# Kernel optimization log

Measured on AMD Instinct MI355X. Metric: run time of the kernel, lower is better.

Reference implementation:

```python
import jax, jax.numpy as jnp
import numpy as np
from jax import lax

# ---- config (matches init_kwargs / detectron2-style inference defaults) ----
B, R, K = 8, 2000, 80          # images, proposals per image, foreground classes
H, W = 800.0, 1333.0           # image (height, width) used for box clipping
SCORE_THRESH = 0.05
NMS_THRESH = 0.5
M = 2048                        # fixed NMS candidate budget (pre-NMS top_k)
T = 100                         # topk_per_image


def setup_inputs() -> dict:
    key = jax.random.key(0)
    k1, k2, k3, k4, k5 = jax.random.split(key, 5)
    # well-formed proposal boxes (x1, y1, x2, y2)
    cx = jax.random.uniform(k1, (B, R)) * W
    cy = jax.random.uniform(k2, (B, R)) * H
    bw = jax.random.uniform(k3, (B, R)) * 300.0 + 2.0
    bh = jax.random.uniform(k4, (B, R)) * 300.0 + 2.0
    boxes = jnp.stack([cx - bw / 2, cy - bh / 2, cx + bw / 2, cy + bh / 2], axis=-1)
    k5a, k5b = jax.random.split(k5)
    scores = jax.random.uniform(k5a, (B, R, K + 1))          # (R, K+1), last col = bg
    bases = jax.random.normal(k5b, (B, R, 7)) * 0.1          # 6 base deltas + 1 h delta
    return {"boxes": boxes.astype(jnp.float32),
            "scores": scores.astype(jnp.float32),
            "bases": bases.astype(jnp.float32)}


def _delta_to_bases(bs, bx):
    # bs: (T, 6) deltas, bx: (T, 4) boxes -> (T, 10) polygon + midpoint
    firstx, firsty = bs[:, 2], bs[:, 3]
    secondx, secondy = bs[:, 4], bs[:, 5]
    x1, y1, x2, y2 = bx[:, 0], bx[:, 1], bx[:, 2], bx[:, 3]
    dx = x2 - x1
    dy = y2 - y1
    midx = (x1 + x2) / 2 + bs[:, 0] * dx
    midy = (y1 + y2) / 2 + bs[:, 1] * dy
    px1 = midx + firstx * dx
    py1 = midy + firsty * dy
    px2 = midx + secondx * dx
    py2 = midy + secondy * dy
    px3 = midx - secondx * dx
    py3 = midy - secondy * dy
    px4 = midx - firstx * dx
    py4 = midy - firsty * dy
    return jnp.stack((px1, py1, px2, py2, px3, py3, px4, py4, midx, midy), axis=-1)


def _delta_to_h(dh, bx):
    dy = bx[:, 3] - bx[:, 1]
    return dy + dh * dy


def _pairwise_iou(b):
    # b: (M, 4). Only used inside a boolean comparison -> no grad path, as in torch NMS.
    x1, y1, x2, y2 = b[:, 0], b[:, 1], b[:, 2], b[:, 3]
    area = jnp.clip(x2 - x1, 0) * jnp.clip(y2 - y1, 0)
    xx1 = jnp.maximum(x1[:, None], x1[None, :])
    yy1 = jnp.maximum(y1[:, None], y1[None, :])
    xx2 = jnp.minimum(x2[:, None], x2[None, :])
    yy2 = jnp.minimum(y2[:, None], y2[None, :])
    inter = jnp.clip(xx2 - xx1, 0) * jnp.clip(yy2 - yy1, 0)
    return inter / (area[:, None] + area[None, :] - inter + 1e-7)


def _single_image(boxes, scores, bases):
    finite = jnp.all(jnp.isfinite(boxes), axis=1) & jnp.all(jnp.isfinite(scores), axis=1)
    scores_k = scores[:, :-1]                                 # drop background (R,K)
    # Boxes.clip(image_shape)
    boxes = jnp.stack([jnp.clip(boxes[:, 0], 0.0, W),
                       jnp.clip(boxes[:, 1], 0.0, H),
                       jnp.clip(boxes[:, 2], 0.0, W),
                       jnp.clip(boxes[:, 3], 0.0, H)], axis=-1)
    # score threshold -> flat (R*K) candidate list, fixed-size top_k selection
    flat = jnp.where(finite[:, None] & (scores_k > SCORE_THRESH), scores_k, -jnp.inf)
    top_scores, top_idx = lax.top_k(flat.reshape(R * K), M)   # (M,)
    box_idx = top_idx // K
    cls = top_idx % K
    cboxes = boxes[box_idx]                                   # (M,4)
    cbases = bases[box_idx]                                   # (M,7)
    valid = jnp.isfinite(top_scores)
    # batched_nms: offset boxes per class so cross-class IoU = 0
    off = (cls.astype(boxes.dtype) * (jnp.maximum(H, W) + 2.0))[:, None]
    iou = _pairwise_iou(cboxes + off)                         # (M,M)

    def body(i, st):
        keep, supp = st
        ki = valid[i] & jnp.logical_not(supp[i])
        keep = keep.at[i].set(ki)
        supp = supp | (ki & (iou[i] > NMS_THRESH))
        return keep, supp

    keep, _ = lax.fori_loop(0, M, body,
                            (jnp.zeros((M,), bool), jnp.zeros((M,), bool)))
    masked = jnp.where(keep, top_scores, -jnp.inf)
    fscores, sel = lax.top_k(masked, T)                       # keep[:topk_per_image]
    fvalid = jnp.isfinite(fscores)
    fscores = jnp.where(fvalid, fscores, 0.0)
    fboxes = cboxes[sel] * fvalid[:, None]
    fbases = cbases[sel]
    fcls = jnp.where(fvalid, cls[sel], -1)
    h = _delta_to_h(fbases[:, 6], fboxes) * fvalid            # (T,)
    dec = _delta_to_bases(fbases[:, 0:6], fboxes) * fvalid[:, None]  # (T,10)
    return dec, h, fboxes, fscores, fcls, fvalid


def reference(boxes, scores, bases):
    # returns per-image padded detections:
    # pred_bases (B,T,10), pred_h (B,T), pred_boxes (B,T,4), scores (B,T),
    # pred_classes (B,T) int, valid mask (B,T)
    return jax.vmap(_single_image)(boxes, scores, bases)
```

## Files before the change

kernel.cpp:

```cpp
#include <hip/hip_runtime.h>
#include <stdint.h>

using u64 = unsigned long long;
using u32 = unsigned;

namespace {
constexpr int RR = 2000;
constexpr int KK = 80;
constexpr int KS = 81;
constexpr int BB = 8;
constexpr int MM = 2048;
constexpr int TT = 100;
constexpr int NB = 2048;
constexpr int CAP = 4096;
constexpr int SPLIT = 50;
constexpr int RPB = RR / SPLIT;
constexpr int FPB = RPB * KS;
constexpr int V4  = FPB / 4;
constexpr int CPB = RPB * KK;
constexpr int SPLIT_H = 10;
constexpr int RPB_H = RR / SPLIT_H;
constexpr int FPB_H = RPB_H * KS;
constexpr int V4_H  = FPB_H / 4;
constexpr float WW  = 1333.0f;
constexpr float HH  = 800.0f;
constexpr float OFF = 1335.0f;
constexpr float STH = 0.05f;
constexpr float NMS = 0.5f;

constexpr size_t HIST_OFF   = 0;
constexpr size_t CNT_OFF    = 65536;
constexpr size_t ZERO_BYTES = 65568;
constexpr size_t CSTAR_OFF  = 65568;
constexpr size_t ROWOK_OFF  = 65664;
constexpr size_t CAND_OFF   = 81920;
}

__global__ __launch_bounds__(1024) void k_hist(const float* __restrict__ boxes,
                                               const float* __restrict__ scores,
                                               u32* __restrict__ hist_g,
                                               unsigned char* __restrict__ rowok_g) {
    const int b = blockIdx.x / SPLIT_H, sb = blockIdx.x % SPLIT_H, tid = threadIdx.x;
    const int r0 = sb * RPB_H;
    const float4* sv = (const float4*)(scores + (size_t)b * RR * KS + (size_t)r0 * KS);
    __shared__ u32 bad[RPB_H];
    __shared__ u32 h[NB];

    const int q0 = tid, q1 = tid + 1024, q2 = tid + 2048, q3 = tid + 3072;
    const float4 v0 = sv[q0];
    const float4 v1 = sv[q1];
    const float4 v2 = sv[q2];
    const float4 v3 = (q3 < V4_H) ? sv[q3] : make_float4(0.f, 0.f, 0.f, 0.f);

    if (tid < RPB_H) bad[tid] = 0;
    for (int i = tid; i < NB; i += 1024) h[i] = 0;
    __syncthreads();

    if (tid < RPB_H) {
        const float4 bx = ((const float4*)(boxes + (size_t)b * RR * 4))[r0 + tid];
        if (!(isfinite(bx.x) && isfinite(bx.y) && isfinite(bx.z) && isfinite(bx.w)))
            atomicOr(&bad[tid], 1u);
    }
    auto chk = [&](int q, const float4& v) {
        if (q < V4_H) {
            const int i0 = 4 * q;
            if (!isfinite(v.x)) atomicOr(&bad[(i0    ) / KS], 1u);
            if (!isfinite(v.y)) atomicOr(&bad[(i0 + 1) / KS], 1u);
            if (!isfinite(v.z)) atomicOr(&bad[(i0 + 2) / KS], 1u);
            if (!isfinite(v.w)) atomicOr(&bad[(i0 + 3) / KS], 1u);
        }
    };
    chk(q0, v0); chk(q1, v1); chk(q2, v2); chk(q3, v3);
    __syncthreads();
    if (tid < RPB_H) rowok_g[b * RR + r0 + tid] = bad[tid] ? 0 : 1;

    auto acc = [&](int idx, float s) {
        const int r_l = idx / KS, k = idx - r_l * KS;
        if (k < KK && bad[r_l] == 0 && s > STH) {
            int bk = (int)(s * (float)NB);
            bk = min(max(bk, 0), NB - 1);
            atomicAdd(&h[bk], 1u);
        }
    };
    auto accv = [&](int q, const float4& v) {
        if (q < V4_H) {
            const int i0 = 4 * q;
            acc(i0, v.x); acc(i0 + 1, v.y); acc(i0 + 2, v.z); acc(i0 + 3, v.w);
        }
    };
    accv(q0, v0); accv(q1, v1); accv(q2, v2); accv(q3, v3);
    __syncthreads();
    for (int i = tid; i < NB; i += 1024)
        if (h[i]) atomicAdd(&hist_g[b * NB + i], h[i]);
}

__global__ __launch_bounds__(256) void k_cut(const u32* __restrict__ hist_g,
                                             u32* __restrict__ cstar_g) {
    const int b = blockIdx.x, tid = threadIdx.x;
    __shared__ u32 h[NB];
    __shared__ u32 cs[256];
    __shared__ u32 cstar_s;
    for (int i = tid; i < NB; i += 256) h[i] = hist_g[b * NB + i];
    if (tid == 0) cstar_s = 0;
    __syncthreads();

    u32 loc[8];
    const int hi = NB - 1 - 8 * tid;
    u32 sum = 0;
#pragma unroll
    for (int j = 0; j < 8; ++j) { loc[j] = h[hi - j]; sum += loc[j]; }
    cs[tid] = sum;
    __syncthreads();
    for (int s = 1; s < 256; s <<= 1) {
        const u32 t = (tid >= s) ? cs[tid - s] : 0u;
        __syncthreads();
        cs[tid] += t;
        __syncthreads();
    }
    const u32 P = cs[tid], Pm1 = (tid > 0) ? cs[tid - 1] : 0u;
    if (P >= (u32)MM && Pm1 < (u32)MM) {
        u32 run = Pm1;
#pragma unroll
        for (int j = 0; j < 8; ++j) {
            run += loc[j];
            if (run >= (u32)MM) { cstar_s = (u32)(hi - j); break; }
        }
    }
    __syncthreads();
    if (tid == 0) cstar_g[b] = cstar_s;
}

__global__ __launch_bounds__(256) void k_compact(const float* __restrict__ scores,
                                                 const u32* __restrict__ cstar_g,
                                                 const unsigned char* __restrict__ rowok_g,
                                                 u64* __restrict__ cand,
                                                 u32* __restrict__ cnt_g) {
    const int b = blockIdx.x / SPLIT, sb = blockIdx.x % SPLIT, tid = threadIdx.x;
    const int r0 = sb * RPB;
    const float4* sv = (const float4*)(scores + (size_t)b * RR * KS + (size_t)r0 * KS);
    __shared__ u64 stage[CPB];
    __shared__ u32 rok[RPB];
    __shared__ u32 scnt, base_s;
    if (tid < RPB) rok[tid] = rowok_g[b * RR + r0 + tid];
    if (tid == 0) scnt = 0;
    __syncthreads();
    const u32 cstar = cstar_g[b];

    auto put = [&](int idx, float s) {
        const int r_l = idx / KS, k = idx - r_l * KS;
        if (k < KK && rok[r_l] && s > STH) {
            int bk = (int)(s * (float)NB);
            bk = min(max(bk, 0), NB - 1);
            if ((u32)bk >= cstar) {
                const u32 p = atomicAdd(&scnt, 1u);
                const u32 eg = (u32)((r0 + r_l) * KK + k);
                stage[p] = ((u64)__float_as_uint(s) << 32) | (u32)(~eg);
            }
        }
    };
#pragma unroll
    for (int it = 0; it < 4; ++it) {
        const int q = tid + it * 256;
        if (q < V4) {
            const float4 v = sv[q];
            const int i0 = 4 * q;
            put(i0, v.x); put(i0 + 1, v.y); put(i0 + 2, v.z); put(i0 + 3, v.w);
        }
    }
    __syncthreads();
    if (tid == 0) base_s = atomicAdd(&cnt_g[b], scnt);
    __syncthreads();
    const u32 base = base_s, nn = scnt;
    u64* cb = cand + (size_t)b * CAP;
    for (u32 i = tid; i < nn; i += 256) {
        const u32 pos = base + i;
        if (pos < (u32)CAP) cb[pos] = stage[i];
    }
}

__device__ __forceinline__ void cmpsw(u64& a, u64& b, bool desc) {
    const u64 mx = a > b ? a : b, mn = a > b ? b : a;
    a = desc ? mx : mn;
    b = desc ? mn : mx;
}
template <unsigned KQ, unsigned JQ>
__device__ __forceinline__ void shfl_stage(u64 (&val)[4], int lane) {
#pragma unroll
    for (int r = 0; r < 4; ++r) {
        const unsigned v = (unsigned)(r * 64 + lane);
        const u64 pv = __shfl_xor(val[r], (int)JQ, 64);
        const bool keepmax = (((v & KQ) == 0) == (((unsigned)lane & JQ) == 0));
        val[r] = keepmax ? (val[r] > pv ? val[r] : pv)
                         : (val[r] < pv ? val[r] : pv);
    }
}

__global__ __launch_bounds__(1024) void k_sort_nms(const float* __restrict__ boxes,
                                                   const float* __restrict__ bases,
                                                   const u64* __restrict__ cand,
                                                   const u32* __restrict__ cnt_g,
                                                   float* __restrict__ out) {
#pragma clang fp contract(off)
    const int b = blockIdx.x, tid = threadIdx.x;
    const int lane = tid & 63;

    __shared__ u64 gk[CAP];
    __shared__ u32 bh[NB];
    __shared__ u32 cs[256];
    __shared__ float4 kbox[TT];
    __shared__ float  karea[TT];
    __shared__ u64    kkey[TT];
    __shared__ int    kcnt_s;

    const u32 n = min(cnt_g[b], (u32)CAP);
    const u64* cb = cand + (size_t)b * CAP;

    u64 myk[4]; int mi[4];
#pragma unroll
    for (int t = 0; t < 4; ++t) {
        mi[t] = tid + t * 1024;
        myk[t] = (mi[t] < (int)n) ? cb[mi[t]] : 0ull;
    }
    for (int i = tid; i < NB; i += 1024) bh[i] = 0;
    if (tid == 0) kcnt_s = 0;
    __syncthreads();

#pragma unroll
    for (int t = 0; t < 4; ++t) {
        if (mi[t] < (int)n) {
            const float s = __uint_as_float((u32)(myk[t] >> 32));
            int bk = (int)(s * (float)NB);
            bk = min(max(bk, 0), NB - 1);
            atomicAdd(&bh[bk], 1u);
        }
    }
    __syncthreads();

    u32 loc[8]; int hi = 0;
    if (tid < 256) {
        hi = NB - 1 - 8 * tid;
        u32 sum = 0;
#pragma unroll
        for (int j = 0; j < 8; ++j) { loc[j] = bh[hi - j]; sum += loc[j]; }
        cs[tid] = sum;
    }
    __syncthreads();
    for (int s = 1; s < 256; s <<= 1) {
        u32 t = 0;
        if (tid < 256 && tid >= s) t = cs[tid - s];
        __syncthreads();
        if (tid < 256) cs[tid] += t;
        __syncthreads();
    }
    if (tid < 256) {
        u32 run = (tid > 0) ? cs[tid - 1] : 0u;
#pragma unroll
        for (int j = 0; j < 8; ++j) { bh[hi - j] = run; run += loc[j]; }
    }
    __syncthreads();

#pragma unroll
    for (int t = 0; t < 4; ++t) {
        if (mi[t] < (int)n) {
            const float s = __uint_as_float((u32)(myk[t] >> 32));
            int bk = (int)(s * (float)NB);
            bk = min(max(bk, 0), NB - 1);
            const u32 pos = atomicAdd(&bh[bk], 1u);
            gk[pos] = myk[t];
        }
    }
    __syncthreads();

    if (tid < 64) {
        const float* bxp = boxes + (size_t)b * RR * 4;
        int kcnt = 0;
        int e = 0, bb = NB - 1;
        while (kcnt < TT && e < (int)n && e < MM) {
            int cend = e;
            while (bb >= 0) {
                const int bend = (int)bh[bb];
                if (bend - e <= 256) { cend = bend; --bb; if (bend - e == 256) break; }
                else break;
            }
            if (cend == e) {
                cend = min(e + 256, (int)bh[bb >= 0 ? bb : 0]); --bb;
            }
            const int csz = cend - e;

            u64 val[4];
#pragma unroll
            for (int r = 0; r < 4; ++r) {
                const int v = r * 64 + lane;
                val[r] = (v < csz) ? gk[e + v] : 0ull;
            }
            shfl_stage<2, 1>(val, lane);
            shfl_stage<4, 2>(val, lane);  shfl_stage<4, 1>(val, lane);
            shfl_stage<8, 4>(val, lane);  shfl_stage<8, 2>(val, lane);  shfl_stage<8, 1>(val, lane);
            shfl_stage<16, 8>(val, lane); shfl_stage<16, 4>(val, lane);
            shfl_stage<16, 2>(val, lane); shfl_stage<16, 1>(val, lane);
            shfl_stage<32, 16>(val, lane); shfl_stage<32, 8>(val, lane);
            shfl_stage<32, 4>(val, lane);  shfl_stage<32, 2>(val, lane); shfl_stage<32, 1>(val, lane);
            shfl_stage<64, 32>(val, lane); shfl_stage<64, 16>(val, lane);
            shfl_stage<64, 8>(val, lane);  shfl_stage<64, 4>(val, lane);
            shfl_stage<64, 2>(val, lane);  shfl_stage<64, 1>(val, lane);
            cmpsw(val[0], val[1], true);   cmpsw(val[2], val[3], false);
            shfl_stage<128, 32>(val, lane); shfl_stage<128, 16>(val, lane);
            shfl_stage<128, 8>(val, lane);  shfl_stage<128, 4>(val, lane);
            shfl_stage<128, 2>(val, lane);  shfl_stage<128, 1>(val, lane);
            cmpsw(val[0], val[2], true);   cmpsw(val[1], val[3], true);
            cmpsw(val[0], val[1], true);   cmpsw(val[2], val[3], true);
            shfl_stage<256, 32>(val, lane); shfl_stage<256, 16>(val, lane);
            shfl_stage<256, 8>(val, lane);  shfl_stage<256, 4>(val, lane);
            shfl_stage<256, 2>(val, lane);  shfl_stage<256, 1>(val, lane);

            float4 bx4[4]; float ar4[4];
#pragma unroll
            for (int r = 0; r < 4; ++r) {
                const u64 key = val[r];
                if ((u32)(key >> 32) != 0u) {
                    const u32 idx = ~(u32)key;
                    const int rr = (int)(idx / KK), cls = (int)(idx - rr * KK);
                    const float x1 = fminf(fmaxf(bxp[rr * 4 + 0], 0.f), WW);
                    const float y1 = fminf(fmaxf(bxp[rr * 4 + 1], 0.f), HH);
                    const float x2 = fminf(fmaxf(bxp[rr * 4 + 2], 0.f), WW);
                    const float y2 = fminf(fmaxf(bxp[rr * 4 + 3], 0.f), HH);
                    const float off = (float)cls * OFF;
                    const float ox1 = x1 + off, oy1 = y1 + off;
                    const float ox2 = x2 + off, oy2 = y2 + off;
                    bx4[r] = make_float4(ox1, oy1, ox2, oy2);
                    ar4[r] = fmaxf(ox2 - ox1, 0.f) * fmaxf(oy2 - oy1, 0.f);
                } else {
                    bx4[r] = make_float4(0.f, 0.f, 0.f, 0.f);
                    ar4[r] = 0.f;
                }
            }

#pragma unroll
            for (int w = 0; w < 4; ++w) {
                if (kcnt >= TT || w * 64 >= csz) break;
                const int rank = e + w * 64 + lane;
                bool undecided = (((u32)(val[w] >> 32)) != 0u) && (rank < MM);
                const float4 box = bx4[w];
                const float  area = ar4[w];
                if (__ballot(undecided) == 0ull) continue;
                for (int kk = 0; kk < kcnt; ++kk) {
                    const float4 kb = kbox[kk];
                    const float  ka = karea[kk];
                    if (undecided) {
                        const float xx1 = fmaxf(kb.x, box.x), yy1 = fmaxf(kb.y, box.y);
                        const float xx2 = fminf(kb.z, box.z), yy2 = fminf(kb.w, box.w);
                        const float inter = fmaxf(xx2 - xx1, 0.f) * fmaxf(yy2 - yy1, 0.f);
                        const float iou = inter / (ka + area - inter + 1e-7f);
                        if (iou > NMS) undecided = false;
                    }
                }
                while (kcnt < TT) {
                    const u64 m = __ballot(undecided);
                    if (m == 0ull) break;
                    const int l = __ffsll((long long)m) - 1;
                    const float bxx = __shfl(box.x, l), byy = __shfl(box.y, l);
                    const float bzz = __shfl(box.z, l), bww = __shfl(box.w, l);
                    const float ba  = __shfl(area,  l);
                    if (lane == l) {
                        undecided = false;
                        kbox[kcnt]  = box;
                        karea[kcnt] = area;
                        kkey[kcnt]  = val[w];
                    }
                    ++kcnt;
                    if (undecided && lane > l) {
                        const float xx1 = fmaxf(bxx, box.x), yy1 = fmaxf(byy, box.y);
                        const float xx2 = fminf(bzz, box.z), yy2 = fminf(bww, box.w);
                        const float inter = fmaxf(xx2 - xx1, 0.f) * fmaxf(yy2 - yy1, 0.f);
                        const float iou = inter / (ba + area - inter + 1e-7f);
                        if (iou > NMS) undecided = false;
                    }
                }
            }
            e = cend;
        }
        if (lane == 0) kcnt_s = kcnt;
    }
    __syncthreads();

    if (tid < TT) {
        const int t = tid;
        const float* bx = boxes + (size_t)b * RR * 4;
        const float* bs = bases + (size_t)b * RR * 7;
        float dec[10] = {0,0,0,0,0,0,0,0,0,0};
        float hval = 0.f, fb0 = 0.f, fb1 = 0.f, fb2 = 0.f, fb3 = 0.f;
        float fs = 0.f, fc = -1.f, fv = 0.f;
        if (t < kcnt_s) {
            const u64 key = kkey[t];
            fs = __uint_as_float((u32)(key >> 32));
            const u32 idx = ~(u32)key;
            const int r = idx / KK, cls = idx - r * KK;
            const float x1 = fminf(fmaxf(bx[r * 4 + 0], 0.f), WW);
            const float y1 = fminf(fmaxf(bx[r * 4 + 1], 0.f), HH);
            const float x2 = fminf(fmaxf(bx[r * 4 + 2], 0.f), WW);
            const float y2 = fminf(fmaxf(bx[r * 4 + 3], 0.f), HH);
            const float* bp = bs + (size_t)r * 7;
            const float b0 = bp[0], b1 = bp[1], b2v = bp[2], b3v = bp[3];
            const float b4 = bp[4], b5 = bp[5], dh = bp[6];
            const float dx = x2 - x1, dy = y2 - y1;
            const float midx = (x1 + x2) / 2.0f + b0 * dx;
            const float midy = (y1 + y2) / 2.0f + b1 * dy;
            dec[0] = midx + b2v * dx; dec[1] = midy + b3v * dy;
            dec[2] = midx + b4  * dx; dec[3] = midy + b5  * dy;
            dec[4] = midx - b4  * dx; dec[5] = midy - b5  * dy;
            dec[6] = midx - b2v * dx; dec[7] = midy - b3v * dy;
            dec[8] = midx; dec[9] = midy;
            hval = dy + dh * dy;
            fb0 = x1; fb1 = y1; fb2 = x2; fb3 = y2;
            fc = (float)cls; fv = 1.f;
        }
        const size_t bt = (size_t)b * TT + t;
        float* dec_o  = out;
        float* h_o    = out + (size_t)BB * TT * 10;
        float* fbox_o = h_o + (size_t)BB * TT;
        float* fsc_o  = fbox_o + (size_t)BB * TT * 4;
        float* fcls_o = fsc_o + (size_t)BB * TT;
        float* fv_o   = fcls_o + (size_t)BB * TT;
        for (int c = 0; c < 10; ++c) dec_o[bt * 10 + c] = dec[c];
        h_o[bt] = hval;
        fbox_o[bt * 4 + 0] = fb0; fbox_o[bt * 4 + 1] = fb1;
        fbox_o[bt * 4 + 2] = fb2; fbox_o[bt * 4 + 3] = fb3;
        fsc_o[bt] = fs;
        fcls_o[bt] = fc;
        fv_o[bt] = fv;
    }
}

extern "C" void kernel_launch(void* const* d_in, const int* in_sizes, int n_in,
                              void* d_out, int out_size, void* d_ws, size_t ws_size,
                              hipStream_t stream) {
    const float* boxes  = (const float*)d_in[0];
    const float* scores = (const float*)d_in[1];
    const float* bases  = (const float*)d_in[2];
    float* out = (float*)d_out;

    char* ws = (char*)d_ws;
    u32* hist_g  = (u32*)(ws + HIST_OFF);
    u32* cnt_g   = (u32*)(ws + CNT_OFF);
    u32* cstar_g = (u32*)(ws + CSTAR_OFF);
    unsigned char* rowok_g = (unsigned char*)(ws + ROWOK_OFF);
    u64* cand    = (u64*)(ws + CAND_OFF);

    hipMemsetAsync(ws, 0, ZERO_BYTES, stream);
    hipLaunchKernelGGL(k_hist,     dim3(BB * SPLIT_H), dim3(1024), 0, stream,
                       boxes, scores, hist_g, rowok_g);
    hipLaunchKernelGGL(k_cut,      dim3(BB),           dim3(256),  0, stream,
                       hist_g, cstar_g);
    hipLaunchKernelGGL(k_compact,  dim3(BB * SPLIT),   dim3(256),  0, stream,
                       scores, cstar_g, rowok_g, cand, cnt_g);
    hipLaunchKernelGGL(k_sort_nms, dim3(BB),           dim3(1024), 0, stream,
                       boxes, bases, cand, cnt_g, out);
}
```

Measured before the change: 120.3 us.

## Precompute intra-wavefront IoU bitmask for greedy NMS within each 64-candidate chunk

Greedy NMS inside each 64-candidate wavefront chunk previously ran one serial step per kept box, each step doing five shuffles plus an IoU evaluation. Now each lane stages its box in shared memory and computes a 64-bit mask of earlier lanes it overlaps. Each serial step then needs only one ballot of that mask. The box loads move into the per-chunk loop instead of being hoisted for all four chunks. The cost is 64 IoU divisions per lane per chunk, run even when few candidates survive, and the branch that skips already-dead lanes against kept boxes is removed.

```diff
diff --git a/kernel.cpp b/kernel.cpp
--- a/kernel.cpp
+++ b/kernel.cpp
@@ -210,6 +210,8 @@
     __shared__ float4 kbox[TT];
     __shared__ float  karea[TT];
     __shared__ u64    kkey[TT];
+    __shared__ float4 wbox[64];
+    __shared__ float  warea[64];
     __shared__ int    kcnt_s;
 
     const u32 n = min(cnt_g[b], (u32)CAP);
@@ -313,11 +315,15 @@
             shfl_stage<256, 8>(val, lane);  shfl_stage<256, 4>(val, lane);
             shfl_stage<256, 2>(val, lane);  shfl_stage<256, 1>(val, lane);
 
-            float4 bx4[4]; float ar4[4];
-#pragma unroll
-            for (int r = 0; r < 4; ++r) {
-                const u64 key = val[r];
-                if ((u32)(key >> 32) != 0u) {
+#pragma unroll 1
+            for (int w = 0; w < 4; ++w) {
+                if (kcnt >= TT || w * 64 >= csz) break;
+                const u64 key = val[w];
+                const int rank = e + w * 64 + lane;
+                const bool valid = (((u32)(key >> 32)) != 0u) && (rank < MM);
+
+                float4 box; float area;
+                if (valid) {
                     const u32 idx = ~(u32)key;
                     const int rr = (int)(idx / KK), cls = (int)(idx - rr * KK);
                     const float x1 = fminf(fmaxf(bxp[rr * 4 + 0], 0.f), WW);
@@ -327,54 +333,51 @@
                     const float off = (float)cls * OFF;
                     const float ox1 = x1 + off, oy1 = y1 + off;
                     const float ox2 = x2 + off, oy2 = y2 + off;
-                    bx4[r] = make_float4(ox1, oy1, ox2, oy2);
-                    ar4[r] = fmaxf(ox2 - ox1, 0.f) * fmaxf(oy2 - oy1, 0.f);
+                    box = make_float4(ox1, oy1, ox2, oy2);
+                    area = fmaxf(ox2 - ox1, 0.f) * fmaxf(oy2 - oy1, 0.f);
                 } else {
-                    bx4[r] = make_float4(0.f, 0.f, 0.f, 0.f);
-                    ar4[r] = 0.f;
+                    box = make_float4(0.f, 0.f, 0.f, 0.f);
+                    area = 0.f;
                 }
-            }
-
-#pragma unroll
-            for (int w = 0; w < 4; ++w) {
-                if (kcnt >= TT || w * 64 >= csz) break;
-                const int rank = e + w * 64 + lane;
-                bool undecided = (((u32)(val[w] >> 32)) != 0u) && (rank < MM);
-                const float4 box = bx4[w];
-                const float  area = ar4[w];
-                if (__ballot(undecided) == 0ull) continue;
+
+                bool alive = valid;
+#pragma unroll 4
                 for (int kk = 0; kk < kcnt; ++kk) {
                     const float4 kb = kbox[kk];
                     const float  ka = karea[kk];
-                    if (undecided) {
-                        const float xx1 = fmaxf(kb.x, box.x), yy1 = fmaxf(kb.y, box.y);
-                        const float xx2 = fminf(kb.z, box.z), yy2 = fminf(kb.w, box.w);
-                        const float inter = fmaxf(xx2 - xx1, 0.f) * fmaxf(yy2 - yy1, 0.f);
-                        const float iou = inter / (ka + area - inter + 1e-7f);
-                        if (iou > NMS) undecided = false;
-                    }
+                    const float xx1 = fmaxf(kb.x, box.x), yy1 = fmaxf(kb.y, box.y);
+                    const float xx2 = fminf(kb.z, box.z), yy2 = fminf(kb.w, box.w);
+                    const float inter = fmaxf(xx2 - xx1, 0.f) * fmaxf(yy2 - yy1, 0.f);
+                    const float iou = inter / (ka + area - inter + 1e-7f);
+                    if (iou > NMS) alive = false;
                 }
-                while (kcnt < TT) {
-                    const u64 m = __ballot(undecided);
-                    if (m == 0ull) break;
-                    const int l = __ffsll((long long)m) - 1;
-                    const float bxx = __shfl(box.x, l), byy = __shfl(box.y, l);
-                    const float bzz = __shfl(box.z, l), bww = __shfl(box.w, l);
-                    const float ba  = __shfl(area,  l);
+
+                wbox[lane] = box;
+                warea[lane] = area;
+                u64 msk = 0;
+#pragma unroll 4
+                for (int i = 0; i < 64; ++i) {
+                    const float4 ib = wbox[i];
+                    const float  ia = warea[i];
+                    const float xx1 = fmaxf(ib.x, box.x), yy1 = fmaxf(ib.y, box.y);
+                    const float xx2 = fminf(ib.z, box.z), yy2 = fminf(ib.w, box.w);
+                    const float inter = fmaxf(xx2 - xx1, 0.f) * fmaxf(yy2 - yy1, 0.f);
+                    const float iou = inter / (ia + area - inter + 1e-7f);
+                    msk |= (iou > NMS ? 1ull : 0ull) << i;
+                }
+                msk &= (lane == 0) ? 0ull : ((1ull << lane) - 1ull);
+
+                u64 und = __ballot(alive);
+                while (und != 0ull && kcnt < TT) {
+                    const int l = __ffsll((long long)und) - 1;
                     if (lane == l) {
-                        undecided = false;
                         kbox[kcnt]  = box;
                         karea[kcnt] = area;
-                        kkey[kcnt]  = val[w];
+                        kkey[kcnt]  = key;
                     }
+                    const u64 supby = __ballot(((msk >> l) & 1ull) != 0ull);
+                    und &= ~(supby | (1ull << (unsigned)l));
                     ++kcnt;
-                    if (undecided && lane > l) {
-                        const float xx1 = fmaxf(bxx, box.x), yy1 = fmaxf(byy, box.y);
-                        const float xx2 = fminf(bzz, box.z), yy2 = fminf(bww, box.w);
-                        const float inter = fmaxf(xx2 - xx1, 0.f) * fmaxf(yy2 - yy1, 0.f);
-                        const float iou = inter / (ba + area - inter + 1e-7f);
-                        if (iou > NMS) undecided = false;
-                    }
                 }
             }
             e = cend;
```

Measured after the change: 113.9 us. 1.06x faster.
